# Kernel tuning notes

Measured on AMD Instinct MI355X. Metric: run time of the kernel, lower is better.

## Reference

```python
import jax, jax.numpy as jnp
import numpy as np

B, N, D = 16, 2048, 256  # batch (pairs*2), num_keypoints, descriptor_dim


def setup_inputs() -> dict:
    key = jax.random.key(0)
    k1, k2, k3, k4 = jax.random.split(key, 4)
    descriptors = jax.random.normal(k1, (B, N, D), dtype=jnp.float32)
    mask = jax.random.randint(k2, (B, N), 0, 2, dtype=jnp.int32)
    proj_w = jax.random.normal(k3, (D, D), dtype=jnp.float32) * 0.02
    proj_b = jnp.zeros((D,), dtype=jnp.float32)
    match_w = jax.random.normal(k4, (1, D), dtype=jnp.float32) * 0.02
    match_b = jnp.zeros((1,), dtype=jnp.float32)
    return {"descriptors": descriptors, "mask": mask, "proj_w": proj_w,
            "proj_b": proj_b, "match_w": match_w, "match_b": match_b}


def reference(descriptors, mask, proj_w, proj_b, match_w, match_b):
    batch, n, d = descriptors.shape
    pairs = batch // 2
    # final projection + temperature scaling
    m_desc = (descriptors @ proj_w.T + proj_b) / jnp.asarray(d, descriptors.dtype) ** 0.25
    m_desc = m_desc.reshape(pairs, 2, n, d)
    # similarity: [pairs, n0, n1]
    similarity = jnp.einsum('bnd,bmd->bnm', m_desc[:, 0], m_desc[:, 1])
    mask_p = mask.reshape(pairs, 2, n)
    pair_mask = mask_p[:, 0][:, :, None] * mask_p[:, 1][:, None, :]
    neg_min = jnp.finfo(similarity.dtype).min
    similarity = jnp.where(pair_mask == 0, neg_min, similarity)
    # matchability logits: [B, n, 1] -> split per pair
    matchability = (descriptors @ match_w.T + match_b).reshape(pairs, 2, n)
    m0 = matchability[:, 0]  # [pairs, n]
    m1 = matchability[:, 1]  # [pairs, n]
    certainties = jax.nn.log_sigmoid(m0)[:, :, None] + jax.nn.log_sigmoid(m1)[:, None, :]
    scores0 = jax.nn.log_softmax(similarity, axis=2)
    scores1 = jax.nn.log_softmax(similarity, axis=1)
    inner = scores0 + scores1 + certainties
    scores = jnp.zeros((pairs, n + 1, n + 1), dtype=similarity.dtype)
    scores = scores.at[:, :n, :n].set(inner)
    scores = scores.at[:, :-1, -1].set(jax.nn.log_sigmoid(-m0))
    scores = scores.at[:, -1, :-1].set(jax.nn.log_sigmoid(-m1))
    return scores
```

## Files before the change

### kernel.cpp

```cpp
#include <hip/hip_runtime.h>
#include <math.h>

typedef unsigned short u16;
typedef __attribute__((ext_vector_type(8))) short bf16x8;
typedef __attribute__((ext_vector_type(4))) float f32x4;

#define N 2048
#define D 256
#define PAIRS 8
#define NO 2049
#define NEGMIN  -3.40282347e38f
#define MASKVAL -3.0e38f
#define LDA 72

#define WS_LS0   0
#define WS_LS1   (1*PAIRS*N)
#define WS_LSN0  (2*PAIRS*N)
#define WS_LSN1  (3*PAIRS*N)
#define WS_RMAX  (4*PAIRS*N)
#define WS_RLSE  (5*PAIRS*N)
#define WS_CMAX  (6*PAIRS*N)
#define WS_CLSE  (7*PAIRS*N)
#define WS_RPM   (8*PAIRS*N)
#define WS_RPS   (WS_RPM + PAIRS*16*N)
#define WS_CPM   (WS_RPS + PAIRS*16*N)
#define WS_CPS   (WS_CPM + PAIRS*16*N)
#define WS_F_COUNT (WS_CPS + PAIRS*16*N)

__device__ __forceinline__ float b2f(u16 u) {
    return __uint_as_float(((unsigned)u) << 16);
}
__device__ __forceinline__ u16 f2b(float f) {
    unsigned x = __float_as_uint(f);
    x += 0x7FFFu + ((x >> 16) & 1u);
    return (u16)(x >> 16);
}
__device__ __forceinline__ unsigned pk2(float a, float b) {
    return (unsigned)f2b(a) | ((unsigned)f2b(b) << 16);
}
__device__ __forceinline__ float logsig(float x) {
    return fminf(x, 0.f) - log1pf(expf(-fabsf(x)));
}
__device__ __forceinline__ void online1(float& m, float& s, float x) {
    float nm = fmaxf(m, x);
    float e = __expf(fminf(m, x) - nm);
    s = (x > m) ? s * e + 1.f : s + e;
    m = nm;
}
__device__ __forceinline__ void onmerge(float& m, float& s, float om, float os) {
    float nm = fmaxf(m, om);
    s = s * __expf(m - nm) + os * __expf(om - nm);
    m = nm;
}

__global__ __launch_bounds__(256) void k_proj_mfma(const float* __restrict__ A,
                                                   const float* __restrict__ W,
                                                   const float* __restrict__ bias,
                                                   const float* __restrict__ mw,
                                                   const float* __restrict__ mb,
                                                   u16* __restrict__ mdesc,
                                                   float* __restrict__ wsf) {
    __shared__ u16 As[128 * LDA];
    __shared__ u16 Bs[128 * LDA];
    int r0 = blockIdx.x * 128, c0 = blockIdx.y * 128;
    int tid = threadIdx.x;
    int w = tid >> 6, lane = tid & 63;
    int ln = lane & 15, q = lane >> 4;
    int wr0 = (w >> 1) * 64, wc0 = (w & 1) * 64;
    f32x4 zero = {0.f, 0.f, 0.f, 0.f};
    f32x4 acc[4][4];
    #pragma unroll
    for (int a = 0; a < 4; ++a)
        #pragma unroll
        for (int b = 0; b < 4; ++b) acc[a][b] = zero;
    float mdot[4] = {0.f, 0.f, 0.f, 0.f};
    int domatch = (blockIdx.y == 0);

    for (int kb = 0; kb < D; kb += 64) {
        __syncthreads();
        #pragma unroll
        for (int t = 0; t < 4; ++t) {
            int c = t * 256 + tid;
            int row = c >> 3, part = c & 7;
            const float* ap = A + (size_t)(r0 + row) * D + kb + part * 8;
            float4 f0 = *(const float4*)ap;
            float4 f1 = *(const float4*)(ap + 4);
            uint4 va;
            va.x = pk2(f0.x, f0.y); va.y = pk2(f0.z, f0.w);
            va.z = pk2(f1.x, f1.y); va.w = pk2(f1.z, f1.w);
            *(uint4*)&As[row * LDA + part * 8] = va;
            if (domatch) {
                float4 w0 = *(const float4*)(mw + kb + part * 8);
                float4 w1 = *(const float4*)(mw + kb + part * 8 + 4);
                mdot[t] += f0.x*w0.x + f0.y*w0.y + f0.z*w0.z + f0.w*w0.w
                         + f1.x*w1.x + f1.y*w1.y + f1.z*w1.z + f1.w*w1.w;
            }
            const float* bp = W + (size_t)(c0 + row) * D + kb + part * 8;
            float4 g0 = *(const float4*)bp;
            float4 g1 = *(const float4*)(bp + 4);
            uint4 vb;
            vb.x = pk2(g0.x, g0.y); vb.y = pk2(g0.z, g0.w);
            vb.z = pk2(g1.x, g1.y); vb.w = pk2(g1.z, g1.w);
            *(uint4*)&Bs[row * LDA + part * 8] = vb;
        }
        __syncthreads();
        #pragma unroll
        for (int kk = 0; kk < 64; kk += 32) {
            bf16x8 af[4], bf[4];
            #pragma unroll
            for (int ri = 0; ri < 4; ++ri)
                af[ri] = *(const bf16x8*)&As[(wr0 + ri*16 + ln) * LDA + kk + q*8];
            #pragma unroll
            for (int ci = 0; ci < 4; ++ci)
                bf[ci] = *(const bf16x8*)&Bs[(wc0 + ci*16 + ln) * LDA + kk + q*8];
            #pragma unroll
            for (int ri = 0; ri < 4; ++ri)
                #pragma unroll
                for (int ci = 0; ci < 4; ++ci)
                    acc[ri][ci] = __builtin_amdgcn_mfma_f32_16x16x32_bf16(af[ri], bf[ci], acc[ri][ci], 0, 0, 0);
        }
    }
    if (domatch) {
        #pragma unroll
        for (int t = 0; t < 4; ++t) {
            float s = mdot[t];
            s += __shfl_xor(s, 1, 64);
            s += __shfl_xor(s, 2, 64);
            s += __shfl_xor(s, 4, 64);
            if ((tid & 7) == 0) {
                int row_g = r0 + t * 32 + (tid >> 3);
                float m = s + mb[0];
                int b = row_g >> 11;
                int i = row_g & (N - 1);
                int pp = b >> 1, sid = b & 1;
                float ls = logsig(m), lsn = logsig(-m);
                if (sid == 0) { wsf[WS_LS0 + pp*N + i] = ls; wsf[WS_LSN0 + pp*N + i] = lsn; }
                else          { wsf[WS_LS1 + pp*N + i] = ls; wsf[WS_LSN1 + pp*N + i] = lsn; }
            }
        }
    }
    #pragma unroll
    for (int ri = 0; ri < 4; ++ri) {
        #pragma unroll
        for (int reg = 0; reg < 4; ++reg) {
            int row = r0 + wr0 + ri*16 + q*4 + reg;
            #pragma unroll
            for (int ci = 0; ci < 4; ++ci) {
                int col = c0 + wc0 + ci*16 + ln;
                float v = (acc[ri][ci][reg] + bias[col]) * 0.25f;
                mdesc[(size_t)row * D + col] = f2b(v);
            }
        }
    }
}

__global__ __launch_bounds__(256) void k_sim_mfma(const u16* __restrict__ mdesc,
                                                  const int* __restrict__ mask,
                                                  u16* __restrict__ out,
                                                  float* __restrict__ wsf) {
    __shared__ u16 As[128 * LDA];
    __shared__ u16 Bs[128 * LDA];
    __shared__ float rpm[128][2], rps[128][2];
    __shared__ float cpm[128][2], cps[128][2];
    int p = blockIdx.z;
    const u16* A  = mdesc + (size_t)(2*p) * N * D;
    const u16* Bm = mdesc + (size_t)(2*p + 1) * N * D;
    int r0 = blockIdx.x * 128, c0 = blockIdx.y * 128;
    int tid = threadIdx.x;
    int w = tid >> 6, lane = tid & 63;
    int ln = lane & 15, q = lane >> 4;
    int wr0 = (w >> 1) * 64, wc0 = (w & 1) * 64;
    f32x4 zero = {0.f, 0.f, 0.f, 0.f};
    f32x4 acc[4][4];
    #pragma unroll
    for (int a = 0; a < 4; ++a)
        #pragma unroll
        for (int b = 0; b < 4; ++b) acc[a][b] = zero;

    for (int kb = 0; kb < D; kb += 64) {
        __syncthreads();
        #pragma unroll
        for (int t = 0; t < 4; ++t) {
            int c = t * 256 + tid;
            int row = c >> 3, part = c & 7;
            uint4 va = *(const uint4*)(A  + (size_t)(r0 + row) * D + kb + part * 8);
            *(uint4*)&As[row * LDA + part * 8] = va;
            uint4 vb = *(const uint4*)(Bm + (size_t)(c0 + row) * D + kb + part * 8);
            *(uint4*)&Bs[row * LDA + part * 8] = vb;
        }
        __syncthreads();
        #pragma unroll
        for (int kk = 0; kk < 64; kk += 32) {
            bf16x8 af[4], bf[4];
            #pragma unroll
            for (int ri = 0; ri < 4; ++ri)
                af[ri] = *(const bf16x8*)&As[(wr0 + ri*16 + ln) * LDA + kk + q*8];
            #pragma unroll
            for (int ci = 0; ci < 4; ++ci)
                bf[ci] = *(const bf16x8*)&Bs[(wc0 + ci*16 + ln) * LDA + kk + q*8];
            #pragma unroll
            for (int ri = 0; ri < 4; ++ri)
                #pragma unroll
                for (int ci = 0; ci < 4; ++ci)
                    acc[ri][ci] = __builtin_amdgcn_mfma_f32_16x16x32_bf16(af[ri], bf[ci], acc[ri][ci], 0, 0, 0);
        }
    }
    const int* m0 = mask + (size_t)(2*p) * N;
    const int* m1 = mask + (size_t)(2*p + 1) * N;
    u16* outp = out + (size_t)p * NO * NO;
    int mcol[4];
    #pragma unroll
    for (int ci = 0; ci < 4; ++ci) mcol[ci] = m1[c0 + wc0 + ci*16 + ln];
    #pragma unroll
    for (int ri = 0; ri < 4; ++ri) {
        #pragma unroll
        for (int reg = 0; reg < 4; ++reg) {
            int row = r0 + wr0 + ri*16 + q*4 + reg;
            int mr = m0[row];
            size_t base = (size_t)row * NO + c0 + wc0 + ln;
            #pragma unroll
            for (int ci = 0; ci < 4; ++ci) {
                float v = (mr && mcol[ci]) ? acc[ri][ci][reg] : MASKVAL;
                acc[ri][ci][reg] = v;
                outp[base + ci*16] = f2b(v);
            }
        }
    }
    #pragma unroll
    for (int ri = 0; ri < 4; ++ri) {
        #pragma unroll
        for (int reg = 0; reg < 4; ++reg) {
            float m = acc[ri][0][reg], s = 1.f;
            online1(m, s, acc[ri][1][reg]);
            online1(m, s, acc[ri][2][reg]);
            online1(m, s, acc[ri][3][reg]);
            #pragma unroll
            for (int off = 1; off <= 8; off <<= 1) {
                float om = __shfl_xor(m, off, 64);
                float os = __shfl_xor(s, off, 64);
                onmerge(m, s, om, os);
            }
            if (ln == 0) {
                int rl = wr0 + ri*16 + q*4 + reg;
                rpm[rl][w & 1] = m; rps[rl][w & 1] = s;
            }
        }
    }
    #pragma unroll
    for (int ci = 0; ci < 4; ++ci) {
        float m = acc[0][ci][0], s = 1.f;
        #pragma unroll
        for (int ri = 0; ri < 4; ++ri)
            #pragma unroll
            for (int reg = 0; reg < 4; ++reg)
                if (!(ri == 0 && reg == 0)) online1(m, s, acc[ri][ci][reg]);
        #pragma unroll
        for (int off = 16; off <= 32; off <<= 1) {
            float om = __shfl_xor(m, off, 64);
            float os = __shfl_xor(s, off, 64);
            onmerge(m, s, om, os);
        }
        if (q == 0) {
            int cl = wc0 + ci*16 + ln;
            cpm[cl][w >> 1] = m; cps[cl][w >> 1] = s;
        }
    }
    __syncthreads();
    if (tid < 128) {
        float m = rpm[tid][0], s = rps[tid][0];
        onmerge(m, s, rpm[tid][1], rps[tid][1]);
        size_t o = (size_t)(p * 16 + blockIdx.y) * N + r0 + tid;
        wsf[WS_RPM + o] = m; wsf[WS_RPS + o] = s;
    } else {
        int c = tid - 128;
        float m = cpm[c][0], s = cps[c][0];
        onmerge(m, s, cpm[c][1], cps[c][1]);
        size_t o = (size_t)(p * 16 + blockIdx.x) * N + c0 + c;
        wsf[WS_CPM + o] = m; wsf[WS_CPS + o] = s;
    }
}

__global__ __launch_bounds__(256) void k_red(float* __restrict__ wsf) {
    int i = blockIdx.x * 256 + threadIdx.x;
    int p = blockIdx.y;
    float m = wsf[WS_CPM + (size_t)(p*16) * N + i];
    float s = wsf[WS_CPS + (size_t)(p*16) * N + i];
    for (int rb = 1; rb < 16; ++rb)
        onmerge(m, s, wsf[WS_CPM + (size_t)(p*16 + rb) * N + i],
                      wsf[WS_CPS + (size_t)(p*16 + rb) * N + i]);
    wsf[WS_CMAX + p * N + i] = m;
    wsf[WS_CLSE + p * N + i] = logf(s);
}

__global__ __launch_bounds__(256) void k_final(u16* __restrict__ out,
                                               const float* __restrict__ wsf) {
    int strip = blockIdx.x;
    int p = blockIdx.y;
    int tid = threadIdx.x;
    __shared__ float rm_l[8], rl_l[8], l0_l[8], ln0_l[8];
    if (tid < 128) {
        int r = tid >> 4, cb = tid & 15;
        int i = strip * 8 + r;
        if (i < N) {
            float m = wsf[WS_RPM + (size_t)(p*16 + cb) * N + i];
            float sv = wsf[WS_RPS + (size_t)(p*16 + cb) * N + i];
            #pragma unroll
            for (int off = 1; off <= 8; off <<= 1) {
                float om = __shfl_xor(m, off, 64);
                float os = __shfl_xor(sv, off, 64);
                onmerge(m, sv, om, os);
            }
            if (cb == 0) {
                rm_l[r]  = m;
                rl_l[r]  = logf(sv);
                l0_l[r]  = wsf[WS_LS0  + p*N + i];
                ln0_l[r] = wsf[WS_LSN0 + p*N + i];
            }
        }
    }
    __syncthreads();
    unsigned* up = (unsigned*)out;
    #pragma unroll
    for (int k = 0; k < 4; ++k) {
        int kk = k * 256 + tid;
        int jc = 2 * kk;
        float cm0 = wsf[WS_CMAX + p*N + jc];
        float cl0 = wsf[WS_CLSE + p*N + jc];
        float s10 = wsf[WS_LS1  + p*N + jc];
        float cm1 = wsf[WS_CMAX + p*N + jc + 1];
        float cl1 = wsf[WS_CLSE + p*N + jc + 1];
        float s11 = wsf[WS_LS1  + p*N + jc + 1];
        float cm2 = 0.f, cl2 = 0.f, s12 = 0.f;
        if (jc + 2 < N) {
            cm2 = wsf[WS_CMAX + p*N + jc + 2];
            cl2 = wsf[WS_CLSE + p*N + jc + 2];
            s12 = wsf[WS_LS1  + p*N + jc + 2];
        }
        for (int r = 0; r < 8; ++r) {
            int i = strip * 8 + r;
            if (i > N) break;
            size_t B0 = ((size_t)p * NO + i) * NO;
            int head = (p + i) & 1;
            size_t U0 = (B0 + head) >> 1;
            if (i == N) {
                int j0 = 2*kk + head;
                float o0 = (j0 < N) ? wsf[WS_LSN1 + p*N + j0] : 0.f;
                int j1 = j0 + 1;
                float o1 = (j1 < N) ? wsf[WS_LSN1 + p*N + j1] : 0.f;
                up[U0 + kk] = pk2(o0, o1);
                if (tid == 0 && k == 0) {
                    if (head) out[B0] = f2b(wsf[WS_LSN1 + p*N]);
                    else      out[B0 + N] = 0;
                }
                continue;
            }
            float rm = rm_l[r], rl = rl_l[r], l0 = l0_l[r], ln0 = ln0_l[r];
            unsigned v = up[U0 + kk];
            float cmA = head ? cm1 : cm0;
            float clA = head ? cl1 : cl0;
            float s1A = head ? s11 : s10;
            float x0 = b2f((u16)v);
            float a0 = (x0 - rm) - rl;
            float b0 = (x0 - cmA) - clA;
            float o0 = fmaxf(fmaxf(a0 + b0, MASKVAL) + (l0 + s1A), MASKVAL);
            float o1;
            int j1 = 2*kk + head + 1;
            if (j1 < N) {
                float cmB = head ? cm2 : cm1;
                float clB = head ? cl2 : cl1;
                float s1B = head ? s12 : s11;
                float x1 = b2f((u16)(v >> 16));
                float a1 = (x1 - rm) - rl;
                float b1 = (x1 - cmB) - clB;
                o1 = fmaxf(fmaxf(a1 + b1, MASKVAL) + (l0 + s1B), MASKVAL);
            } else {
                o1 = ln0;
            }
            up[U0 + kk] = pk2(o0, o1);
            if (tid == 0 && k == 0) {
                if (head) {
                    float x = b2f(out[B0]);
                    float a = (x - rm) - rl;
                    float b = (x - wsf[WS_CMAX + p*N]) - wsf[WS_CLSE + p*N];
                    out[B0] = f2b(fmaxf(fmaxf(a + b, MASKVAL) + (l0 + wsf[WS_LS1 + p*N]), MASKVAL));
                } else {
                    out[B0 + N] = f2b(ln0);
                }
            }
        }
    }
}

extern "C" void kernel_launch(void* const* d_in, const int* in_sizes, int n_in,
                              void* d_out, int out_size, void* d_ws, size_t ws_size,
                              hipStream_t stream) {
    const float* desc    = (const float*)d_in[0];
    const int*   mask    = (const int*)d_in[1];
    const float* proj_w  = (const float*)d_in[2];
    const float* proj_b  = (const float*)d_in[3];
    const float* match_w = (const float*)d_in[4];
    const float* match_b = (const float*)d_in[5];
    u16*   out = (u16*)d_out;
    float* wsf = (float*)d_ws;
    u16*   mdesc = (u16*)((char*)d_ws + (size_t)WS_F_COUNT * sizeof(float));

    k_proj_mfma<<<dim3(256, 2),    256, 0, stream>>>(desc, proj_w, proj_b, match_w, match_b, mdesc, wsf);
    k_sim_mfma <<<dim3(16, 16, 8), 256, 0, stream>>>(mdesc, mask, out, wsf);
    k_red      <<<dim3(8, 8),      256, 0, stream>>>(wsf);
    k_final    <<<dim3(257, 8),    256, 0, stream>>>(out, wsf);
}
```

Measured before the change: 257.1 us.

## Stage GEMM outputs through LDS, write similarity to aligned workspace, use direct global-to-LDS loads

```diff
diff --git a/kernel.cpp b/kernel.cpp
--- a/kernel.cpp
+++ b/kernel.cpp
@@ -12,6 +12,7 @@
 #define NEGMIN  -3.40282347e38f
 #define MASKVAL -3.0e38f
 #define LDA 72
+#define LDST 136
 
 #define WS_LS0   0
 #define WS_LS1   (1*PAIRS*N)
@@ -52,6 +53,11 @@
     s = s * __expf(m - nm) + os * __expf(om - nm);
     m = nm;
 }
+__device__ __forceinline__ void gl_lds16(const u16* g, u16* l) {
+    __builtin_amdgcn_global_load_lds(
+        (const __attribute__((address_space(1))) unsigned*)(const void*)g,
+        (__attribute__((address_space(3))) unsigned*)(void*)l, 16, 0, 0);
+}
 
 __global__ __launch_bounds__(256) void k_proj_mfma(const float* __restrict__ A,
                                                    const float* __restrict__ W,
@@ -60,8 +66,10 @@
                                                    const float* __restrict__ mb,
                                                    u16* __restrict__ mdesc,
                                                    float* __restrict__ wsf) {
-    __shared__ u16 As[128 * LDA];
-    __shared__ u16 Bs[128 * LDA];
+    __shared__ union {
+        struct { u16 A[128 * LDA]; u16 B[128 * LDA]; } t;
+        u16 stage[128][LDST];
+    } sh;
     int r0 = blockIdx.x * 128, c0 = blockIdx.y * 128;
     int tid = threadIdx.x;
     int w = tid >> 6, lane = tid & 63;
@@ -88,7 +96,7 @@
             uint4 va;
             va.x = pk2(f0.x, f0.y); va.y = pk2(f0.z, f0.w);
             va.z = pk2(f1.x, f1.y); va.w = pk2(f1.z, f1.w);
-            *(uint4*)&As[row * LDA + part * 8] = va;
+            *(uint4*)&sh.t.A[row * LDA + part * 8] = va;
             if (domatch) {
                 float4 w0 = *(const float4*)(mw + kb + part * 8);
                 float4 w1 = *(const float4*)(mw + kb + part * 8 + 4);
@@ -101,7 +109,7 @@
             uint4 vb;
             vb.x = pk2(g0.x, g0.y); vb.y = pk2(g0.z, g0.w);
             vb.z = pk2(g1.x, g1.y); vb.w = pk2(g1.z, g1.w);
-            *(uint4*)&Bs[row * LDA + part * 8] = vb;
+            *(uint4*)&sh.t.B[row * LDA + part * 8] = vb;
         }
         __syncthreads();
         #pragma unroll
@@ -109,10 +117,10 @@
             bf16x8 af[4], bf[4];
             #pragma unroll
             for (int ri = 0; ri < 4; ++ri)
-                af[ri] = *(const bf16x8*)&As[(wr0 + ri*16 + ln) * LDA + kk + q*8];
+                af[ri] = *(const bf16x8*)&sh.t.A[(wr0 + ri*16 + ln) * LDA + kk + q*8];
             #pragma unroll
             for (int ci = 0; ci < 4; ++ci)
-                bf[ci] = *(const bf16x8*)&Bs[(wc0 + ci*16 + ln) * LDA + kk + q*8];
+                bf[ci] = *(const bf16x8*)&sh.t.B[(wc0 + ci*16 + ln) * LDA + kk + q*8];
             #pragma unroll
             for (int ri = 0; ri < 4; ++ri)
                 #pragma unroll
@@ -139,37 +147,50 @@
             }
         }
     }
+    __syncthreads();
     #pragma unroll
     for (int ri = 0; ri < 4; ++ri) {
         #pragma unroll
         for (int reg = 0; reg < 4; ++reg) {
-            int row = r0 + wr0 + ri*16 + q*4 + reg;
+            int row_l = wr0 + ri*16 + q*4 + reg;
             #pragma unroll
             for (int ci = 0; ci < 4; ++ci) {
                 int col = c0 + wc0 + ci*16 + ln;
                 float v = (acc[ri][ci][reg] + bias[col]) * 0.25f;
-                mdesc[(size_t)row * D + col] = f2b(v);
-            }
-        }
+                sh.stage[row_l][wc0 + ci*16 + ln] = f2b(v);
+            }
+        }
+    }
+    __syncthreads();
+    {
+        int row_l = tid >> 1, half = tid & 1;
+        u16* dp = mdesc + (size_t)(r0 + row_l) * D + c0 + half * 64;
+        const u16* lp = &sh.stage[row_l][half * 64];
+        #pragma unroll
+        for (int i = 0; i < 8; ++i)
+            *(uint4*)(dp + i * 8) = *(const uint4*)(lp + i * 8);
     }
 }
 
 __global__ __launch_bounds__(256) void k_sim_mfma(const u16* __restrict__ mdesc,
                                                   const int* __restrict__ mask,
-                                                  u16* __restrict__ out,
+                                                  u16* __restrict__ sim,
                                                   float* __restrict__ wsf) {
-    __shared__ u16 As[128 * LDA];
-    __shared__ u16 Bs[128 * LDA];
+    __shared__ union {
+        struct { u16 A[128 * 64]; u16 B[128 * 64]; } t;
+        u16 stage[128][LDST];
+    } sh;
     __shared__ float rpm[128][2], rps[128][2];
     __shared__ float cpm[128][2], cps[128][2];
     int p = blockIdx.z;
-    const u16* A  = mdesc + (size_t)(2*p) * N * D;
+    const u16* Am = mdesc + (size_t)(2*p) * N * D;
     const u16* Bm = mdesc + (size_t)(2*p + 1) * N * D;
     int r0 = blockIdx.x * 128, c0 = blockIdx.y * 128;
     int tid = threadIdx.x;
     int w = tid >> 6, lane = tid & 63;
     int ln = lane & 15, q = lane >> 4;
     int wr0 = (w >> 1) * 64, wc0 = (w & 1) * 64;
+    int scol = (lane & 7) * 8;
     f32x4 zero = {0.f, 0.f, 0.f, 0.f};
     f32x4 acc[4][4];
     #pragma unroll
@@ -178,15 +199,11 @@
         for (int b = 0; b < 4; ++b) acc[a][b] = zero;
 
     for (int kb = 0; kb < D; kb += 64) {
-        __syncthreads();
-        #pragma unroll
-        for (int t = 0; t < 4; ++t) {
-            int c = t * 256 + tid;
-            int row = c >> 3, part = c & 7;
-            uint4 va = *(const uint4*)(A  + (size_t)(r0 + row) * D + kb + part * 8);
-            *(uint4*)&As[row * LDA + part * 8] = va;
-            uint4 vb = *(const uint4*)(Bm + (size_t)(c0 + row) * D + kb + part * 8);
-            *(uint4*)&Bs[row * LDA + part * 8] = vb;
+        #pragma unroll
+        for (int j = 0; j < 4; ++j) {
+            int row = w * 32 + j * 8 + (lane >> 3);
+            gl_lds16(Am + (size_t)(r0 + row) * D + kb + scol, &sh.t.A[(w * 32 + j * 8) * 64]);
+            gl_lds16(Bm + (size_t)(c0 + row) * D + kb + scol, &sh.t.B[(w * 32 + j * 8) * 64]);
         }
         __syncthreads();
         #pragma unroll
@@ -194,20 +211,20 @@
             bf16x8 af[4], bf[4];
             #pragma unroll
             for (int ri = 0; ri < 4; ++ri)
-                af[ri] = *(const bf16x8*)&As[(wr0 + ri*16 + ln) * LDA + kk + q*8];
+                af[ri] = *(const bf16x8*)&sh.t.A[(wr0 + ri*16 + ln) * 64 + kk + q*8];
             #pragma unroll
             for (int ci = 0; ci < 4; ++ci)
-                bf[ci] = *(const bf16x8*)&Bs[(wc0 + ci*16 + ln) * LDA + kk + q*8];
+                bf[ci] = *(const bf16x8*)&sh.t.B[(wc0 + ci*16 + ln) * 64 + kk + q*8];
             #pragma unroll
             for (int ri = 0; ri < 4; ++ri)
                 #pragma unroll
                 for (int ci = 0; ci < 4; ++ci)
                     acc[ri][ci] = __builtin_amdgcn_mfma_f32_16x16x32_bf16(af[ri], bf[ci], acc[ri][ci], 0, 0, 0);
         }
+        __syncthreads();
     }
     const int* m0 = mask + (size_t)(2*p) * N;
     const int* m1 = mask + (size_t)(2*p + 1) * N;
-    u16* outp = out + (size_t)p * NO * NO;
     int mcol[4];
     #pragma unroll
     for (int ci = 0; ci < 4; ++ci) mcol[ci] = m1[c0 + wc0 + ci*16 + ln];
@@ -215,14 +232,13 @@
     for (int ri = 0; ri < 4; ++ri) {
         #pragma unroll
         for (int reg = 0; reg < 4; ++reg) {
-            int row = r0 + wr0 + ri*16 + q*4 + reg;
-            int mr = m0[row];
-            size_t base = (size_t)row * NO + c0 + wc0 + ln;
+            int row_l = wr0 + ri*16 + q*4 + reg;
+            int mr = m0[r0 + row_l];
             #pragma unroll
             for (int ci = 0; ci < 4; ++ci) {
                 float v = (mr && mcol[ci]) ? acc[ri][ci][reg] : MASKVAL;
                 acc[ri][ci][reg] = v;
-                outp[base + ci*16] = f2b(v);
+                sh.stage[row_l][wc0 + ci*16 + ln] = f2b(v);
             }
         }
     }
@@ -266,6 +282,14 @@
         }
     }
     __syncthreads();
+    {
+        int row_l = tid >> 1, half = tid & 1;
+        u16* sp = sim + ((size_t)p * N + r0 + row_l) * N + c0 + half * 64;
+        const u16* lp = &sh.stage[row_l][half * 64];
+        #pragma unroll
+        for (int i = 0; i < 8; ++i)
+            *(uint4*)(sp + i * 8) = *(const uint4*)(lp + i * 8);
+    }
     if (tid < 128) {
         float m = rpm[tid][0], s = rps[tid][0];
         onmerge(m, s, rpm[tid][1], rps[tid][1]);
@@ -276,7 +300,8 @@
         float m = cpm[c][0], s = cps[c][0];
         onmerge(m, s, cpm[c][1], cps[c][1]);
         size_t o = (size_t)(p * 16 + blockIdx.x) * N + c0 + c;
-        wsf[WS_CPM + o] = m; wsf[WS_CPS + o] = s;
+        wsf[WS_CPM + o] = m; wsf[WS_CLSE + 0] = wsf[WS_CLSE + 0];
+        wsf[WS_CPS + o] = s;
     }
 }
 
@@ -285,6 +310,7 @@
     int p = blockIdx.y;
     float m = wsf[WS_CPM + (size_t)(p*16) * N + i];
     float s = wsf[WS_CPS + (size_t)(p*16) * N + i];
+    #pragma unroll
     for (int rb = 1; rb < 16; ++rb)
         onmerge(m, s, wsf[WS_CPM + (size_t)(p*16 + rb) * N + i],
                       wsf[WS_CPS + (size_t)(p*16 + rb) * N + i]);
@@ -293,6 +319,7 @@
 }
 
 __global__ __launch_bounds__(256) void k_final(u16* __restrict__ out,
+                                               const u16* __restrict__ sim,
                                                const float* __restrict__ wsf) {
     int strip = blockIdx.x;
     int p = blockIdx.y;
@@ -355,34 +382,39 @@
                 continue;
             }
             float rm = rm_l[r], rl = rl_l[r], l0 = l0_l[r], ln0 = ln0_l[r];
-            unsigned v = up[U0 + kk];
-            float cmA = head ? cm1 : cm0;
-            float clA = head ? cl1 : cl0;
-            float s1A = head ? s11 : s10;
-            float x0 = b2f((u16)v);
-            float a0 = (x0 - rm) - rl;
-            float b0 = (x0 - cmA) - clA;
-            float o0 = fmaxf(fmaxf(a0 + b0, MASKVAL) + (l0 + s1A), MASKVAL);
-            float o1;
-            int j1 = 2*kk + head + 1;
-            if (j1 < N) {
-                float cmB = head ? cm2 : cm1;
-                float clB = head ? cl2 : cl1;
-                float s1B = head ? s12 : s11;
-                float x1 = b2f((u16)(v >> 16));
+            const u16* srow = sim + ((size_t)p * N + i) * N;
+            unsigned a = *(const unsigned*)(srow + jc);
+            float o0, o1;
+            if (head) {
+                float x0 = b2f((u16)(a >> 16));
+                float a0 = (x0 - rm) - rl;
+                float b0 = (x0 - cm1) - cl1;
+                o0 = fmaxf(fmaxf(a0 + b0, MASKVAL) + (l0 + s11), MASKVAL);
+                if (jc + 2 < N) {
+                    float x1 = b2f(srow[jc + 2]);
+                    float a1 = (x1 - rm) - rl;
+                    float b1 = (x1 - cm2) - cl2;
+                    o1 = fmaxf(fmaxf(a1 + b1, MASKVAL) + (l0 + s12), MASKVAL);
+                } else {
+                    o1 = ln0;
+                }
+            } else {
+                float x0 = b2f((u16)a);
+                float a0 = (x0 - rm) - rl;
+                float b0 = (x0 - cm0) - cl0;
+                o0 = fmaxf(fmaxf(a0 + b0, MASKVAL) + (l0 + s10), MASKVAL);
+                float x1 = b2f((u16)(a >> 16));
                 float a1 = (x1 - rm) - rl;
-                float b1 = (x1 - cmB) - clB;
-                o1 = fmaxf(fmaxf(a1 + b1, MASKVAL) + (l0 + s1B), MASKVAL);
-            } else {
-                o1 = ln0;
+                float b1 = (x1 - cm1) - cl1;
+                o1 = fmaxf(fmaxf(a1 + b1, MASKVAL) + (l0 + s11), MASKVAL);
             }
             up[U0 + kk] = pk2(o0, o1);
             if (tid == 0 && k == 0) {
                 if (head) {
-                    float x = b2f(out[B0]);
-                    float a = (x - rm) - rl;
-                    float b = (x - wsf[WS_CMAX + p*N]) - wsf[WS_CLSE + p*N];
-                    out[B0] = f2b(fmaxf(fmaxf(a + b, MASKVAL) + (l0 + wsf[WS_LS1 + p*N]), MASKVAL));
+                    float x = b2f(srow[0]);
+                    float aa = (x - rm) - rl;
+                    float bb = (x - wsf[WS_CMAX + p*N]) - wsf[WS_CLSE + p*N];
+                    out[B0] = f2b(fmaxf(fmaxf(aa + bb, MASKVAL) + (l0 + wsf[WS_LS1 + p*N]), MASKVAL));
                 } else {
                     out[B0 + N] = f2b(ln0);
                 }
@@ -403,9 +435,10 @@
     u16*   out = (u16*)d_out;
     float* wsf = (float*)d_ws;
     u16*   mdesc = (u16*)((char*)d_ws + (size_t)WS_F_COUNT * sizeof(float));
+    u16*   simw  = mdesc + (size_t)16 * N * D;
 
     k_proj_mfma<<<dim3(256, 2),    256, 0, stream>>>(desc, proj_w, proj_b, match_w, match_b, mdesc, wsf);
-    k_sim_mfma <<<dim3(16, 16, 8), 256, 0, stream>>>(mdesc, mask, out, wsf);
+    k_sim_mfma <<<dim3(16, 16, 8), 256, 0, stream>>>(mdesc, mask, simw, wsf);
     k_red      <<<dim3(8, 8),      256, 0, stream>>>(wsf);
-    k_final    <<<dim3(257, 8),    256, 0, stream>>>(out, wsf);
-}
+    k_final    <<<dim3(257, 8),    256, 0, stream>>>(out, simw, wsf);
+}
```

After: 278.4 us. 8.3% more time.
